# Optimization experiments

Measured on AMD Instinct MI355X. Metric: run time of the kernel, lower is better.

## Reference

```python
import jax, jax.numpy as jnp
import numpy as np
from math import sqrt

B, L, H, E = 4, 2048, 16, 64
S, D = 2048, 64

def setup_inputs() -> dict:
    key = jax.random.key(0)
    kq, kk, kv = jax.random.split(key, 3)
    queries = jax.random.normal(kq, (B, L, H, E), dtype=jnp.float32)
    keys = jax.random.normal(kk, (B, S, H, E), dtype=jnp.float32)
    values = jax.random.normal(kv, (B, S, H, D), dtype=jnp.float32)
    return {"queries": queries, "keys": keys, "values": values}

def reference(queries, keys, values):
    Bq, Lq, Hq, Eq = queries.shape
    Sk = keys.shape[1]
    scale = 1.0 / sqrt(Eq)
    # scores: [B, H, L, S]
    scores = jnp.einsum('blhe,bshe->bhls', queries, keys)
    # TriangularCausalMask: mask positions where key index > query index
    causal = jnp.triu(jnp.ones((Lq, Sk), dtype=bool), k=1)  # True above diagonal
    scores = jnp.where(causal, -jnp.inf, scores)
    A = jax.nn.softmax(scale * scores, axis=-1)  # dropout p=0.0 -> identity
    V = jnp.einsum('bhls,bshd->blhd', A, values)
    return V
```

## Files before the change

### kernel.cpp

```cpp
#include <hip/hip_runtime.h>
#include <hip/hip_bf16.h>

typedef __attribute__((ext_vector_type(8))) short short8;
typedef __attribute__((ext_vector_type(4))) short short4v;
typedef __attribute__((ext_vector_type(16))) float f32x16;

constexpr int Bc = 4;
constexpr int Lc = 2048;
constexpr int Sc = 2048;
constexpr int Hc = 16;
constexpr int Ec = 64;
constexpr int Dc = 64;
constexpr int QBLK = 128;
constexpr int KBLK = 64;
constexpr int NQT  = Lc / QBLK;

__device__ __forceinline__ unsigned short b16(float x) {
  __bf16 h = (__bf16)x;
  return __builtin_bit_cast(unsigned short, h);
}
__device__ __forceinline__ unsigned pk2(float lo, float hi) {
  return (unsigned)b16(lo) | ((unsigned)b16(hi) << 16);
}
__device__ __forceinline__ short8 cvt8(float4 a, float4 b) {
  short8 w;
  w[0] = (short)b16(a.x); w[1] = (short)b16(a.y);
  w[2] = (short)b16(a.z); w[3] = (short)b16(a.w);
  w[4] = (short)b16(b.x); w[5] = (short)b16(b.y);
  w[6] = (short)b16(b.z); w[7] = (short)b16(b.w);
  return w;
}
__device__ __forceinline__ short8 mk8(unsigned d0, unsigned d1, unsigned d2, unsigned d3) {
  union { unsigned u[4]; short8 s; } t;
  t.u[0] = d0; t.u[1] = d1; t.u[2] = d2; t.u[3] = d3;
  return t.s;
}
__device__ __forceinline__ float max3f(float a, float b, float c) {
  return fmaxf(fmaxf(a, b), c);
}

struct KV { float4 k[4]; float4 v[4]; };

__global__ __launch_bounds__(256, 2)
void fattn_kernel(const float* __restrict__ Qg, const float* __restrict__ Kg,
                  const float* __restrict__ Vg, float* __restrict__ Og) {
  __shared__ unsigned short Kl[2][KBLK * 64];
  __shared__ unsigned short Vl[2][KBLK * 64];

  const int tid  = (int)threadIdx.x;
  const int wave = tid >> 6;
  const int lane = tid & 63;
  const int q32  = lane & 31;
  const int hi   = lane >> 5;

  const int bh = (int)blockIdx.x;
  const int pb = (int)blockIdx.y;
  const int b  = bh >> 4;
  const int h  = bh & 15;

  const int qA   = pb;
  const int qB   = NQT - 1 - pb;
  const int q0A  = qA * QBLK + wave * 32;
  const int q0B  = qB * QBLK + wave * 32;
  const int nchA = 2 * pb + 2;
  const int nchB = 2 * qB + 2;

  const float QSCALE = 0.125f * 1.44269504088896341f;
  auto loadQ = [&](int q0, short8 (&qf)[4]) {
    const float* qp = Qg + (((size_t)(b * Lc + q0 + q32)) * Hc + h) * Ec;
#pragma unroll
    for (int c = 0; c < 4; ++c) {
      const float4* p4 = (const float4*)(qp + c * 16 + hi * 8);
      float4 x = p4[0], y = p4[1];
      x.x *= QSCALE; x.y *= QSCALE; x.z *= QSCALE; x.w *= QSCALE;
      y.x *= QSCALE; y.y *= QSCALE; y.z *= QSCALE; y.w *= QSCALE;
      qf[c] = cvt8(x, y);
    }
  };
  short8 qfA[4], qfB[4];
  loadQ(q0A, qfA);
  loadQ(q0B, qfB);

  short8 ones;
#pragma unroll
  for (int j = 0; j < 8; ++j) ones[j] = (short)0x3F80;

  const int s  = tid >> 2;
  const int e0 = (tid & 3) << 4;

  auto loadKV = [&](int ch) {
    KV r;
    const size_t row = (((size_t)(b * Sc + ch * KBLK + s)) * Hc + h);
    const float4* kp4 = (const float4*)(Kg + row * Ec + e0);
    const float4* vp4 = (const float4*)(Vg + row * Dc + e0);
#pragma unroll
    for (int i = 0; i < 4; ++i) { r.k[i] = kp4[i]; r.v[i] = vp4[i]; }
    return r;
  };

  auto writeKV = [&](const KV& r, int buf) {
    short8 w0 = cvt8(r.k[0], r.k[1]);
    short8 w1 = cvt8(r.k[2], r.k[3]);
    const int c0 = e0 >> 3;
    *(short8*)&Kl[buf][s * 64 + (((c0    ) ^ (s & 7)) << 3)] = w0;
    *(short8*)&Kl[buf][s * 64 + (((c0 + 1) ^ (s & 7)) << 3)] = w1;
    short8 wv0 = cvt8(r.v[0], r.v[1]);
    short8 wv1 = cvt8(r.v[2], r.v[3]);
    const int vt = ((s >> 2) * 4 + (tid & 3)) * 64 + (s & 3) * 16;
    *(short8*)&Vl[buf][vt]     = wv0;
    *(short8*)&Vl[buf][vt + 8] = wv1;
  };

  f32x16 accoA0 = (f32x16)(0.f), accoA1 = (f32x16)(0.f), acclA = (f32x16)(0.f);
  f32x16 accoB0 = (f32x16)(0.f), accoB1 = (f32x16)(0.f), acclB = (f32x16)(0.f);
  float mA = -1e30f, mB = -1e30f;

  auto doTile = [&](int ch, int cur, int q0w, const short8 (&qf)[4],
                    f32x16& acco0, f32x16& acco1, f32x16& accl, float& m_run) {
    const int s0 = ch * 64;
    const bool act0 = (s0 <= q0w);
    if (!act0) return;
    const bool act1  = (s0 + 32 <= q0w);
    const bool diag0 = (s0 == q0w);
    const bool diag1 = (s0 + 32 == q0w);

    auto qk = [&](int sb) {
      f32x16 acc = (f32x16)(0.f);
      const int sr = sb * 32 + q32;
      const int rb = sr * 64;
      const int sw = sr & 7;
#pragma unroll
      for (int c = 0; c < 4; ++c) {
        short8 kf = *(const short8*)&Kl[cur][rb + (((2 * c + hi) ^ sw) << 3)];
        acc = __builtin_amdgcn_mfma_f32_32x32x16_bf16(kf, qf[c], acc, 0, 0, 0);
      }
      return acc;
    };
    f32x16 S0 = qk(0);
    f32x16 S1;
    if (act1) S1 = qk(1);

    const int tq = q32 - 4 * hi;
    if (diag0) {
#pragma unroll
      for (int r = 0; r < 16; ++r)
        if (((r & 3) + 8 * (r >> 2)) > tq) S0[r] = -1e30f;
    }
    if (act1 && diag1) {
#pragma unroll
      for (int r = 0; r < 16; ++r)
        if (((r & 3) + 8 * (r >> 2)) > tq) S1[r] = -1e30f;
    }

    float pmax;
    {
      float t0 = max3f(S0[0],  S0[1],  S0[2]);
      float t1 = max3f(S0[3],  S0[4],  S0[5]);
      float t2 = max3f(S0[6],  S0[7],  S0[8]);
      float t3 = max3f(S0[9],  S0[10], S0[11]);
      float t4 = max3f(S0[12], S0[13], S0[14]);
      float u0 = max3f(t0, t1, t2);
      float u1 = max3f(t3, t4, S0[15]);
      pmax = fmaxf(u0, u1);
      if (act1) {
        float v0 = max3f(S1[0],  S1[1],  S1[2]);
        float v1 = max3f(S1[3],  S1[4],  S1[5]);
        float v2 = max3f(S1[6],  S1[7],  S1[8]);
        float v3 = max3f(S1[9],  S1[10], S1[11]);
        float v4 = max3f(S1[12], S1[13], S1[14]);
        float w0 = max3f(v0, v1, v2);
        float w1 = max3f(v3, v4, S1[15]);
        pmax = max3f(pmax, w0, w1);
      }
    }
    {
      unsigned px = __builtin_bit_cast(unsigned, pmax);
      auto sw = __builtin_amdgcn_permlane32_swap(px, px, false, false);
      pmax = fmaxf(__builtin_bit_cast(float, (unsigned)sw[0]),
                   __builtin_bit_cast(float, (unsigned)sw[1]));
    }

    if (!__all(pmax - m_run <= 8.0f)) {
      const float mnew  = fmaxf(m_run, pmax);
      const float alpha = exp2f(m_run - mnew);
      m_run = mnew;
      const int hib = hi << 4;
      const int av  = __builtin_bit_cast(int, alpha);
#pragma unroll
      for (int r = 0; r < 16; ++r) {
        const int addr = hib + 4 * ((r & 3) + 8 * (r >> 2));
        float ar = __builtin_bit_cast(float, __builtin_amdgcn_ds_bpermute(addr, av));
        acco0[r] *= ar; acco1[r] *= ar; accl[r] *= ar;
      }
    }

#pragma unroll
    for (int r = 0; r < 16; ++r) S0[r] = exp2f(S0[r] - m_run);
    if (act1) {
#pragma unroll
      for (int r = 0; r < 16; ++r) S1[r] = exp2f(S1[r] - m_run);
    }

    auto mkpa = [&](const f32x16& P, int a, int bidx) {
      unsigned A0 = pk2(P[4 * a + 0],    P[4 * a + 1]);
      unsigned A1 = pk2(P[4 * a + 2],    P[4 * a + 3]);
      unsigned B0 = pk2(P[4 * bidx + 0], P[4 * bidx + 1]);
      unsigned B1 = pk2(P[4 * bidx + 2], P[4 * bidx + 3]);
      auto r0 = __builtin_amdgcn_permlane32_swap(A0, B0, false, false);
      auto r1 = __builtin_amdgcn_permlane32_swap(A1, B1, false, false);
      return mk8((unsigned)r0[0], (unsigned)r1[0], (unsigned)r0[1], (unsigned)r1[1]);
    };
    short8 pa0 = mkpa(S0, 0, 1);
    short8 pa1 = mkpa(S0, 2, 3);
    short8 pa2, pa3;
    if (act1) { pa2 = mkpa(S1, 0, 1); pa3 = mkpa(S1, 2, 3); }

    const unsigned vbase = (unsigned)(size_t)(&Vl[cur][0]);
    const unsigned vcol  = ((unsigned)(q32 & 15) << 3);
    short4v vlo[2][4], vhi[2][4];
#pragma unroll
    for (int dt = 0; dt < 2; ++dt) {
#pragma unroll
      for (int ks = 0; ks < 4; ++ks) {
        if (ks < 2 || act1) {
          const unsigned a0 = vbase +
            ((((unsigned)(4 * ks + 2 * hi) * 4u) + 2u * dt + (unsigned)(q32 >> 4)) << 7) + vcol;
          asm volatile("ds_read_b64_tr_b16 %0, %1 offset:0"   : "=&v"(vlo[dt][ks]) : "v"(a0));
          asm volatile("ds_read_b64_tr_b16 %0, %1 offset:512" : "=&v"(vhi[dt][ks]) : "v"(a0));
        }
      }
    }

    accl = __builtin_amdgcn_mfma_f32_32x32x16_bf16(pa0, ones, accl, 0, 0, 0);
    accl = __builtin_amdgcn_mfma_f32_32x32x16_bf16(pa1, ones, accl, 0, 0, 0);
    if (act1) {
      accl = __builtin_amdgcn_mfma_f32_32x32x16_bf16(pa2, ones, accl, 0, 0, 0);
      accl = __builtin_amdgcn_mfma_f32_32x32x16_bf16(pa3, ones, accl, 0, 0, 0);
    }

    if (act1) { asm volatile("s_waitcnt lgkmcnt(8)" ::: "memory"); }
    else      { asm volatile("s_waitcnt lgkmcnt(4)" ::: "memory"); }
    __builtin_amdgcn_sched_barrier(0);

    __builtin_amdgcn_s_setprio(1);
    {
      f32x16& ac = acco0;
      short8 vf0 = __builtin_shufflevector(vlo[0][0], vhi[0][0], 0,1,2,3,4,5,6,7);
      short8 vf1 = __builtin_shufflevector(vlo[0][1], vhi[0][1], 0,1,2,3,4,5,6,7);
      ac = __builtin_amdgcn_mfma_f32_32x32x16_bf16(pa0, vf0, ac, 0, 0, 0);
      ac = __builtin_amdgcn_mfma_f32_32x32x16_bf16(pa1, vf1, ac, 0, 0, 0);
      if (act1) {
        short8 vf2 = __builtin_shufflevector(vlo[0][2], vhi[0][2], 0,1,2,3,4,5,6,7);
        short8 vf3 = __builtin_shufflevector(vlo[0][3], vhi[0][3], 0,1,2,3,4,5,6,7);
        ac = __builtin_amdgcn_mfma_f32_32x32x16_bf16(pa2, vf2, ac, 0, 0, 0);
        ac = __builtin_amdgcn_mfma_f32_32x32x16_bf16(pa3, vf3, ac, 0, 0, 0);
      }
    }
    __builtin_amdgcn_s_setprio(0);

    asm volatile("s_waitcnt lgkmcnt(0)" ::: "memory");
    __builtin_amdgcn_sched_barrier(0);

    __builtin_amdgcn_s_setprio(1);
    {
      f32x16& ac = acco1;
      short8 vf0 = __builtin_shufflevector(vlo[1][0], vhi[1][0], 0,1,2,3,4,5,6,7);
      short8 vf1 = __builtin_shufflevector(vlo[1][1], vhi[1][1], 0,1,2,3,4,5,6,7);
      ac = __builtin_amdgcn_mfma_f32_32x32x16_bf16(pa0, vf0, ac, 0, 0, 0);
      ac = __builtin_amdgcn_mfma_f32_32x32x16_bf16(pa1, vf1, ac, 0, 0, 0);
      if (act1) {
        short8 vf2 = __builtin_shufflevector(vlo[1][2], vhi[1][2], 0,1,2,3,4,5,6,7);
        short8 vf3 = __builtin_shufflevector(vlo[1][3], vhi[1][3], 0,1,2,3,4,5,6,7);
        ac = __builtin_amdgcn_mfma_f32_32x32x16_bf16(pa2, vf2, ac, 0, 0, 0);
        ac = __builtin_amdgcn_mfma_f32_32x32x16_bf16(pa3, vf3, ac, 0, 0, 0);
      }
    }
    __builtin_amdgcn_s_setprio(0);
  };

  { KV r0 = loadKV(0); writeKV(r0, 0); }
  __syncthreads();

  int cur = 0;
  for (int ch = 0; ch < nchB; ++ch) {
    const bool pref = (ch + 1 < nchB);
    KV nxt;
    if (pref) nxt = loadKV(ch + 1);

    doTile(ch, cur, q0B, qfB, accoB0, accoB1, acclB, mB);
    if (ch < nchA) doTile(ch, cur, q0A, qfA, accoA0, accoA1, acclA, mA);

    if (pref) writeKV(nxt, cur ^ 1);
    __syncthreads();
    cur ^= 1;
  }

  auto epi = [&](int q0w, const f32x16& acco0, const f32x16& acco1, const f32x16& accl) {
#pragma unroll
    for (int r = 0; r < 16; ++r) {
      const int q_loc = (r & 3) + 8 * (r >> 2) + 4 * hi;
      const int q = q0w + q_loc;
      const float inv = 1.0f / accl[r];
      float* op = Og + (((size_t)(b * Lc + q)) * Hc + h) * Dc + q32;
      op[0]  = acco0[r] * inv;
      op[32] = acco1[r] * inv;
    }
  };
  epi(q0A, accoA0, accoA1, acclA);
  epi(q0B, accoB0, accoB1, acclB);
}

extern "C" void kernel_launch(void* const* d_in, const int* in_sizes, int n_in,
                              void* d_out, int out_size, void* d_ws, size_t ws_size,
                              hipStream_t stream) {
  const float* Q = (const float*)d_in[0];
  const float* K = (const float*)d_in[1];
  const float* V = (const float*)d_in[2];
  float* O = (float*)d_out;
  dim3 grid(Bc * Hc, NQT / 2);
  fattn_kernel<<<grid, 256, 0, stream>>>(Q, K, V, O);
}
```

Baseline: 95.58 us.

## Replace paired causal q-tile blocks with one q-tile per block

Each block previously handled two query tiles (pb and NQT-1-pb) to balance causal work, sharing each K/V chunk load between them. The kernel now handles a single query tile per block and doubles the grid, with heaviest tiles scheduled first via reversed indexing. This cuts per-block register pressure and improves occupancy and parallelism. The cost is more K/V global loads and bf16 conversions, since chunks are no longer shared across two tiles, plus some load imbalance across blocks.

New measurement: 100.6 us. 1.05x slower.

```diff
diff --git a/kernel.cpp b/kernel.cpp
--- a/kernel.cpp
+++ b/kernel.cpp
@@ -58,16 +58,14 @@
   const int b  = bh >> 4;
   const int h  = bh & 15;
 
-  const int qA   = pb;
-  const int qB   = NQT - 1 - pb;
-  const int q0A  = qA * QBLK + wave * 32;
-  const int q0B  = qB * QBLK + wave * 32;
-  const int nchA = 2 * pb + 2;
-  const int nchB = 2 * qB + 2;
+  const int qtile = NQT - 1 - pb;
+  const int q0w   = qtile * QBLK + wave * 32;
+  const int nch   = 2 * qtile + 2;
 
   const float QSCALE = 0.125f * 1.44269504088896341f;
-  auto loadQ = [&](int q0, short8 (&qf)[4]) {
-    const float* qp = Qg + (((size_t)(b * Lc + q0 + q32)) * Hc + h) * Ec;
+  short8 qf[4];
+  {
+    const float* qp = Qg + (((size_t)(b * Lc + q0w + q32)) * Hc + h) * Ec;
 #pragma unroll
     for (int c = 0; c < 4; ++c) {
       const float4* p4 = (const float4*)(qp + c * 16 + hi * 8);
@@ -76,10 +74,7 @@
       y.x *= QSCALE; y.y *= QSCALE; y.z *= QSCALE; y.w *= QSCALE;
       qf[c] = cvt8(x, y);
     }
-  };
-  short8 qfA[4], qfB[4];
-  loadQ(q0A, qfA);
-  loadQ(q0B, qfB);
+  }
 
   short8 ones;
 #pragma unroll
@@ -111,15 +106,12 @@
     *(short8*)&Vl[buf][vt + 8] = wv1;
   };
 
-  f32x16 accoA0 = (f32x16)(0.f), accoA1 = (f32x16)(0.f), acclA = (f32x16)(0.f);
-  f32x16 accoB0 = (f32x16)(0.f), accoB1 = (f32x16)(0.f), acclB = (f32x16)(0.f);
-  float mA = -1e30f, mB = -1e30f;
-
-  auto doTile = [&](int ch, int cur, int q0w, const short8 (&qf)[4],
-                    f32x16& acco0, f32x16& acco1, f32x16& accl, float& m_run) {
+  f32x16 acco0 = (f32x16)(0.f), acco1 = (f32x16)(0.f), accl = (f32x16)(0.f);
+  float m_run = -1e30f;
+
+  auto doTile = [&](int ch, int cur) {
     const int s0 = ch * 64;
-    const bool act0 = (s0 <= q0w);
-    if (!act0) return;
+    if (s0 > q0w) return;
     const bool act1  = (s0 + 32 <= q0w);
     const bool diag0 = (s0 == q0w);
     const bool diag1 = (s0 + 32 == q0w);
@@ -282,32 +274,27 @@
   __syncthreads();
 
   int cur = 0;
-  for (int ch = 0; ch < nchB; ++ch) {
-    const bool pref = (ch + 1 < nchB);
+  for (int ch = 0; ch < nch; ++ch) {
+    const bool pref = (ch + 1 < nch);
     KV nxt;
     if (pref) nxt = loadKV(ch + 1);
 
-    doTile(ch, cur, q0B, qfB, accoB0, accoB1, acclB, mB);
-    if (ch < nchA) doTile(ch, cur, q0A, qfA, accoA0, accoA1, acclA, mA);
+    doTile(ch, cur);
 
     if (pref) writeKV(nxt, cur ^ 1);
     __syncthreads();
     cur ^= 1;
   }
 
-  auto epi = [&](int q0w, const f32x16& acco0, const f32x16& acco1, const f32x16& accl) {
-#pragma unroll
-    for (int r = 0; r < 16; ++r) {
-      const int q_loc = (r & 3) + 8 * (r >> 2) + 4 * hi;
-      const int q = q0w + q_loc;
-      const float inv = 1.0f / accl[r];
-      float* op = Og + (((size_t)(b * Lc + q)) * Hc + h) * Dc + q32;
-      op[0]  = acco0[r] * inv;
-      op[32] = acco1[r] * inv;
-    }
-  };
-  epi(q0A, accoA0, accoA1, acclA);
-  epi(q0B, accoB0, accoB1, acclB);
+#pragma unroll
+  for (int r = 0; r < 16; ++r) {
+    const int q_loc = (r & 3) + 8 * (r >> 2) + 4 * hi;
+    const int q = q0w + q_loc;
+    const float inv = 1.0f / accl[r];
+    float* op = Og + (((size_t)(b * Lc + q)) * Hc + h) * Dc + q32;
+    op[0]  = acco0[r] * inv;
+    op[32] = acco1[r] * inv;
+  }
 }
 
 extern "C" void kernel_launch(void* const* d_in, const int* in_sizes, int n_in,
@@ -317,6 +304,6 @@
   const float* K = (const float*)d_in[1];
   const float* V = (const float*)d_in[2];
   float* O = (float*)d_out;
-  dim3 grid(Bc * Hc, NQT / 2);
+  dim3 grid(Bc * Hc, NQT);
   fattn_kernel<<<grid, 256, 0, stream>>>(Q, K, V, O);
 }
```
